# Kernel tuning notes

Hardware: AMD Instinct MI355X
Metric: run time of the kernel (lower is better)

## Reference

```python
import jax, jax.numpy as jnp
import numpy as np

DIM = 3072
NUM_HEADS = 24
HEAD_DIM = 128
INNER = NUM_HEADS * HEAD_DIM
EPS = 1e-5


def _layernorm(x, eps=EPS):
    # affine-free LayerNorm over the last (head_dim) axis
    mu = jnp.mean(x, axis=-1, keepdims=True)
    var = jnp.mean(jnp.square(x - mu), axis=-1, keepdims=True)
    return (x - mu) * jax.lax.rsqrt(var + eps)


def _rope_interleaved(x, cos, sin):
    # x: (B, S_img, H, D); cos/sin: (S_img, D//2). Non-neox (interleaved) style.
    x1 = x[..., 0::2]
    x2 = x[..., 1::2]
    c = cos[None, :, None, :]
    s = sin[None, :, None, :]
    o1 = x1 * c - x2 * s
    o2 = x2 * c + x1 * s
    return jnp.stack([o1, o2], axis=-1).reshape(x.shape)


def setup_inputs() -> dict:
    key = jax.random.key(0)
    ks = jax.random.split(key, 8)
    B, S_txt, S_img = 1, 256, 2048
    hidden_states = jax.random.normal(ks[0], (B, S_img, DIM), dtype=jnp.float32)
    encoder_hidden_states = jax.random.normal(ks[1], (B, S_txt, DIM), dtype=jnp.float32)
    cos = jax.random.uniform(ks[2], (S_img, HEAD_DIM // 2), dtype=jnp.float32)
    sin = jax.random.uniform(ks[3], (S_img, HEAD_DIM // 2), dtype=jnp.float32)
    Wqkv = jax.random.normal(ks[4], (DIM, 3 * INNER), dtype=jnp.float32) * (DIM ** -0.5)
    bqkv = jnp.zeros((3 * INNER,), dtype=jnp.float32)
    Wout = jax.random.normal(ks[5], (INNER, DIM), dtype=jnp.float32) * (INNER ** -0.5)
    bout = jnp.zeros((DIM,), dtype=jnp.float32)
    return {
        "hidden_states": hidden_states,
        "encoder_hidden_states": encoder_hidden_states,
        "cos": cos,
        "sin": sin,
        "Wqkv": Wqkv,
        "bqkv": bqkv,
        "Wout": Wout,
        "bout": bout,
        "text_seq_length": 256,
    }


def reference(hidden_states, encoder_hidden_states, cos, sin, Wqkv, bqkv, Wout, bout, text_seq_length):
    T = text_seq_length
    x = jnp.concatenate([encoder_hidden_states, hidden_states], axis=1)  # (B, S, dim)
    B, S, _ = x.shape
    qkv = x @ Wqkv + bqkv  # (B, S, 3*inner)
    q, k, v = jnp.split(qkv, 3, axis=-1)
    q = q.reshape(B, S, NUM_HEADS, HEAD_DIM)
    k = k.reshape(B, S, NUM_HEADS, HEAD_DIM)
    v = v.reshape(B, S, NUM_HEADS, HEAD_DIM)
    q = _layernorm(q)
    k = _layernorm(k)
    # partial RoPE: only on image-token slice
    q = jnp.concatenate([q[:, :T], _rope_interleaved(q[:, T:], cos, sin)], axis=1)
    k = jnp.concatenate([k[:, :T], _rope_interleaved(k[:, T:], cos, sin)], axis=1)
    scale = 1.0 / (HEAD_DIM ** 0.5)
    scores = jnp.einsum("bqhd,bkhd->bhqk", q, k) * scale
    probs = jax.nn.softmax(scores, axis=-1)
    out = jnp.einsum("bhqk,bkhd->bqhd", probs, v)
    out = out.reshape(B, S, INNER)
    out = out @ Wout + bout
    encoder_out = out[:, :T, :]
    hidden_out = out[:, T:, :]
    return (hidden_out, encoder_out)
```

## Files before the change

### kernel.cpp

```cpp
#include <hip/hip_runtime.h>

#define DIMC 3072
#define NH 24
#define HD 128
#define QKV_N 9216
#define S_TXT 256
#define S_IMG 2048
#define S_TOT 2304

typedef _Float16 f16x8 __attribute__((ext_vector_type(8)));
typedef _Float16 f16x4 __attribute__((ext_vector_type(4)));
typedef _Float16 f16x2 __attribute__((ext_vector_type(2)));
typedef float f32x4 __attribute__((ext_vector_type(4)));

#define MFMA(A, B, C) __builtin_amdgcn_mfma_f32_16x16x32_f16(A, B, C, 0, 0, 0)

#define QSCALE (0.08838834764831845f * 1.4426950408889634f)

__device__ __forceinline__ void gl2lds16(const _Float16* g, _Float16* l) {
    __builtin_amdgcn_global_load_lds(
        (const __attribute__((address_space(1))) unsigned int*)g,
        (__attribute__((address_space(3))) unsigned int*)l,
        16, 0, 0);
}

__global__ __launch_bounds__(256) void split_x(
    const float* __restrict__ enc, const float* __restrict__ hid,
    _Float16* __restrict__ xh)
{
    const int s = blockIdx.x;
    const float* src = (s < S_TXT) ? enc + (size_t)s * DIMC
                                   : hid + (size_t)(s - S_TXT) * DIMC;
    const int t = threadIdx.x;
#pragma unroll
    for (int it = 0; it < 3; ++it) {
        const int i = (it * 256 + t) * 4;
        float4 v = *(const float4*)(src + i);
        f16x4 hv;
        hv.x = (_Float16)v.x; hv.y = (_Float16)v.y;
        hv.z = (_Float16)v.z; hv.w = (_Float16)v.w;
        *(f16x4*)(xh + (size_t)s * DIMC + i) = hv;
    }
}

__global__ __launch_bounds__(256) void transpose_w_hi(
    const float* __restrict__ W, const int ldw, _Float16* __restrict__ Th)
{
    __shared__ float T[64][68];
    const int n0 = blockIdx.x * 64, k0 = blockIdx.y * 64;
    const int t = threadIdx.x;
    {
        const int r = t >> 2, c4 = (t & 3) * 16;
#pragma unroll
        for (int j = 0; j < 4; ++j) {
            float4 v = *(const float4*)(W + (size_t)(k0 + r) * ldw + n0 + c4 + j * 4);
            *(float4*)&T[r][c4 + j * 4] = v;
        }
    }
    __syncthreads();
    const int nr = t >> 2, kp = (t & 3) * 16;
    f16x8 hv0, hv1;
#pragma unroll
    for (int j = 0; j < 8; ++j) hv0[j] = (_Float16)T[kp + j][nr];
#pragma unroll
    for (int j = 0; j < 8; ++j) hv1[j] = (_Float16)T[kp + 8 + j][nr];
    _Float16* dh = Th + (size_t)(n0 + nr) * DIMC + k0 + kp;
    *(f16x8*)(dh) = hv0; *(f16x8*)(dh + 8) = hv1;
}

template <int REMAP>
__global__ __launch_bounds__(256) void gemm_f16_lds(
    const _Float16* __restrict__ Ah, const _Float16* __restrict__ Bh,
    const float* __restrict__ bias, float* __restrict__ C,
    const int nblk_m, const int ldc)
{
    __shared__ __attribute__((aligned(16))) _Float16 Ash[128 * 32];
    __shared__ __attribute__((aligned(16))) _Float16 Bsh[128 * 32];

    const int cpx = (int)gridDim.x >> 3;
    const int wgid = (blockIdx.x & 7) * cpx + (blockIdx.x >> 3);
    const int bm = (wgid % nblk_m) * 128;
    const int bn = (wgid / nblk_m) * 128;

    const int tid = threadIdx.x;
    const int l = tid & 63, w = tid >> 6;
    const int wr = w >> 1, wc = w & 1;
    const int lr = l & 15, g = l >> 4;

    const int srow0 = w * 32 + (l >> 2);
    const int srow1 = srow0 + 16;
    const int skp0 = (((l & 3) ^ ((srow0 >> 1) & 3)) * 8);
    const int skp1 = (((l & 3) ^ ((srow1 >> 1) & 3)) * 8);
    const _Float16* gA0 = Ah + (size_t)(bm + srow0) * DIMC + skp0;
    const _Float16* gA1 = Ah + (size_t)(bm + srow1) * DIMC + skp1;
    const _Float16* gB0 = Bh + (size_t)(bn + srow0) * DIMC + skp0;
    const _Float16* gB1 = Bh + (size_t)(bn + srow1) * DIMC + skp1;
    _Float16* lA0 = &Ash[(w * 32) * 32];
    _Float16* lA1 = &Ash[(w * 32 + 16) * 32];
    _Float16* lB0 = &Bsh[(w * 32) * 32];
    _Float16* lB1 = &Bsh[(w * 32 + 16) * 32];

    int aoff[4], boff[4];
#pragma unroll
    for (int i = 0; i < 4; ++i) {
        const int ra = wr * 64 + i * 16 + lr;
        const int rb = wc * 64 + i * 16 + lr;
        aoff[i] = ra * 32 + ((g ^ ((ra >> 1) & 3)) * 8);
        boff[i] = rb * 32 + ((g ^ ((rb >> 1) & 3)) * 8);
    }

    f32x4 acc[4][4] = {};

    for (int k0 = 0; k0 < DIMC; k0 += 32) {
        gl2lds16(gA0 + k0, lA0);
        gl2lds16(gA1 + k0, lA1);
        gl2lds16(gB0 + k0, lB0);
        gl2lds16(gB1 + k0, lB1);
        __syncthreads();

        f16x8 bhf[4];
#pragma unroll
        for (int ni = 0; ni < 4; ++ni)
            bhf[ni] = *(const f16x8*)&Bsh[boff[ni]];
#pragma unroll
        for (int mi = 0; mi < 4; ++mi) {
            f16x8 ahf = *(const f16x8*)&Ash[aoff[mi]];
#pragma unroll
            for (int ni = 0; ni < 4; ++ni)
                acc[mi][ni] = MFMA(ahf, bhf[ni], acc[mi][ni]);
        }
        __syncthreads();
    }

#pragma unroll
    for (int mi = 0; mi < 4; ++mi)
#pragma unroll
        for (int ni = 0; ni < 4; ++ni) {
            const int cl = bn + wc * 64 + ni * 16 + lr;
            const float bv = bias[cl];
#pragma unroll
            for (int e = 0; e < 4; ++e) {
                const int r = bm + wr * 64 + mi * 16 + g * 4 + e;
                if (REMAP) {
                    const int gr = (r < S_TXT) ? (S_IMG + r) : (r - S_TXT);
                    C[(size_t)gr * DIMC + cl] = acc[mi][ni][e] + bv;
                } else {
                    C[(size_t)r * ldc + cl] = acc[mi][ni][e] + bv;
                }
            }
        }
}

__global__ __launch_bounds__(256) void ln_rope_split(
    const float* __restrict__ qkv,
    const float* __restrict__ cost, const float* __restrict__ sint,
    _Float16* __restrict__ Qh, _Float16* __restrict__ Kh)
{
    const int wave = threadIdx.x >> 6;
    const int lane = threadIdx.x & 63;
    const int task = blockIdx.x * 4 + wave;
    const int s = task / 48;
    const int rem = task % 48;
    const int qk = rem / 24;
    const int h = rem % 24;

    const float* p = qkv + (size_t)s * QKV_N + qk * DIMC + h * HD;
    float2 x = *(const float2*)(p + lane * 2);

    float sum = x.x + x.y;
    float sq = x.x * x.x + x.y * x.y;
#pragma unroll
    for (int off = 1; off < 64; off <<= 1) {
        sum += __shfl_xor(sum, off, 64);
        sq  += __shfl_xor(sq, off, 64);
    }
    const float mu = sum * (1.0f / 128.0f);
    const float var = sq * (1.0f / 128.0f) - mu * mu;
    const float rstd = rsqrtf(var + 1e-5f);
    float y0 = (x.x - mu) * rstd;
    float y1 = (x.y - mu) * rstd;

    if (s >= S_TXT) {
        const int ip = s - S_TXT;
        const float c = cost[ip * 64 + lane];
        const float sn = sint[ip * 64 + lane];
        const float o0 = y0 * c - y1 * sn;
        const float o1 = y1 * c + y0 * sn;
        y0 = o0; y1 = o1;
    }
    if (qk == 0) { y0 *= QSCALE; y1 *= QSCALE; }

    const size_t off = ((size_t)h * S_TOT + s) * HD + lane * 2;
    f16x2 hv; hv.x = (_Float16)y0; hv.y = (_Float16)y1;
    *(f16x2*)((qk ? Kh : Qh) + off) = hv;
}

__global__ __launch_bounds__(256) void v_split_transpose(
    const float* __restrict__ qkv, _Float16* __restrict__ Vth)
{
    __shared__ float T[64][132];
    const int h = blockIdx.y;
    const int s0 = blockIdx.x * 64;
    const int t = threadIdx.x;
    {
        const int sl = t >> 2, dp = (t & 3) * 32;
#pragma unroll
        for (int j = 0; j < 8; ++j) {
            float4 v = *(const float4*)(qkv + (size_t)(s0 + sl) * QKV_N + 2 * DIMC + h * HD + dp + j * 4);
            *(float4*)&T[sl][dp + j * 4] = v;
        }
    }
    __syncthreads();
    const int d = t >> 1, sh = (t & 1) * 32;
    f16x8 hv[4];
#pragma unroll
    for (int ss = 0; ss < 32; ++ss)
        hv[ss >> 3][ss & 7] = (_Float16)T[sh + ss][d];
    _Float16* bh = Vth + ((size_t)h * HD + d) * S_TOT + s0 + sh;
#pragma unroll
    for (int j = 0; j < 4; ++j)
        *(f16x8*)(bh + j * 8) = hv[j];
}

__global__ __launch_bounds__(256) void attn_mfma(
    const _Float16* __restrict__ Qg, const _Float16* __restrict__ Kg,
    const _Float16* __restrict__ Vg, _Float16* __restrict__ aoh)
{
    __shared__ __attribute__((aligned(16))) _Float16 Ksh[4 * 64 * 32];
    __shared__ __attribute__((aligned(16))) _Float16 Vsh[128 * 64];
    __shared__ __attribute__((aligned(16))) _Float16 Pah[4 * 16 * 64];

    const int wgid = ((int)blockIdx.x & 7) * 108 + ((int)blockIdx.x >> 3);
    const int h = wgid / 36;
    const int q0 = (wgid % 36) * 64;
    const int tid = threadIdx.x;
    const int w = tid >> 6, l = tid & 63;
    const int lr = l & 15, g = l >> 4;

    const int qrow = q0 + w * 16 + lr;
    const _Float16* qb = Qg + ((size_t)h * S_TOT + qrow) * HD + g * 8;
    f16x8 qh[4];
#pragma unroll
    for (int db = 0; db < 4; ++db)
        qh[db] = *(const f16x8*)(qb + db * 32);

    f32x4 o[8] = {};
    float mrow = -3.0e38f, lrow = 0.0f;

    const int kxr = (lr >> 1) & 3;
    const int px  = lr & 7;
    int ksl[4];
#pragma unroll
    for (int db = 0; db < 4; ++db) ksl[db] = (g ^ kxr ^ db) * 8;
    const int vs0 = (g ^ px) * 8;
    const int vs1 = ((4 + g) ^ px) * 8;

    const int kkv = tid >> 2, kdb = tid & 3;
    const int vd = tid >> 1;
    const int kx = (kkv >> 1) & 3;
    const int kbase = kdb * 2048 + kkv * 32;
    const int vbase = vd * 64;
    const int vx = vd & 7;
    const int vg0 = (tid & 1) * 4;
    const _Float16* gK = Kg + ((size_t)h * S_TOT + kkv) * HD + kdb * 32;
    const _Float16* gV = Vg + ((size_t)h * HD + vd) * S_TOT + (tid & 1) * 32;

    uint4 rK0, rK1, rK2, rK3, rV0, rV1, rV2, rV3;
#define LOADKV(kv0) { \
    rK0 = *(const uint4*)(gK + (size_t)(kv0) * HD);      rK1 = *(const uint4*)(gK + (size_t)(kv0) * HD + 8); \
    rK2 = *(const uint4*)(gK + (size_t)(kv0) * HD + 16); rK3 = *(const uint4*)(gK + (size_t)(kv0) * HD + 24); \
    rV0 = *(const uint4*)(gV + (kv0));      rV1 = *(const uint4*)(gV + (kv0) + 8); \
    rV2 = *(const uint4*)(gV + (kv0) + 16); rV3 = *(const uint4*)(gV + (kv0) + 24); }

    LOADKV(0);

    for (int kb = 0; kb < S_TOT / 64; ++kb) {
        __syncthreads();
        *(uint4*)&Ksh[kbase + ((0 ^ kx ^ kdb) * 8)] = rK0;
        *(uint4*)&Ksh[kbase + ((1 ^ kx ^ kdb) * 8)] = rK1;
        *(uint4*)&Ksh[kbase + ((2 ^ kx ^ kdb) * 8)] = rK2;
        *(uint4*)&Ksh[kbase + ((3 ^ kx ^ kdb) * 8)] = rK3;
        *(uint4*)&Vsh[vbase + (((vg0 + 0) ^ vx) * 8)] = rV0;
        *(uint4*)&Vsh[vbase + (((vg0 + 1) ^ vx) * 8)] = rV1;
        *(uint4*)&Vsh[vbase + (((vg0 + 2) ^ vx) * 8)] = rV2;
        *(uint4*)&Vsh[vbase + (((vg0 + 3) ^ vx) * 8)] = rV3;
        __syncthreads();
        if (kb + 1 < S_TOT / 64) LOADKV((kb + 1) * 64);

        f32x4 sT[4] = {};
        __builtin_amdgcn_s_setprio(1);
#pragma unroll
        for (int db = 0; db < 4; ++db)
#pragma unroll
            for (int mf = 0; mf < 4; ++mf) {
                f16x8 kf = *(const f16x8*)&Ksh[db * 2048 + (mf * 16 + lr) * 32 + ksl[db]];
                sT[mf] = MFMA(kf, qh[db], sT[mf]);
            }
        __builtin_amdgcn_s_setprio(0);

        float pm = -3.0e38f;
#pragma unroll
        for (int mf = 0; mf < 4; ++mf)
#pragma unroll
            for (int e = 0; e < 4; ++e)
                pm = fmaxf(pm, sT[mf][e]);
        pm = fmaxf(pm, __shfl_xor(pm, 16, 64));
        pm = fmaxf(pm, __shfl_xor(pm, 32, 64));

        if (__any(pm > mrow + 11.0f)) {
            const float mnew = fmaxf(mrow, pm);
            const float alpha = exp2f(mrow - mnew);
            lrow *= alpha;
            mrow = mnew;
            const float a0 = __shfl(alpha, g * 4 + 0, 64);
            const float a1 = __shfl(alpha, g * 4 + 1, 64);
            const float a2 = __shfl(alpha, g * 4 + 2, 64);
            const float a3 = __shfl(alpha, g * 4 + 3, 64);
#pragma unroll
            for (int df = 0; df < 8; ++df) {
                o[df][0] *= a0; o[df][1] *= a1; o[df][2] *= a2; o[df][3] *= a3;
            }
        }

        float rs = 0.0f;
        float ex_[4][4];
#pragma unroll
        for (int mf = 0; mf < 4; ++mf)
#pragma unroll
            for (int e = 0; e < 4; ++e) {
                const float pv = exp2f(sT[mf][e] - mrow);
                ex_[mf][e] = pv;
                rs += pv;
            }
        rs += __shfl_xor(rs, 16, 64);
        rs += __shfl_xor(rs, 32, 64);
        lrow += rs;

        {
            const int pbase = w * 1024 + lr * 64;
#pragma unroll
            for (int mf = 0; mf < 4; ++mf) {
                const int slot = ((mf * 2 + (g >> 1)) ^ px) * 8 + (g & 1) * 4;
                f16x2 t0; t0.x = (_Float16)ex_[mf][0]; t0.y = (_Float16)ex_[mf][1];
                f16x2 t1; t1.x = (_Float16)ex_[mf][2]; t1.y = (_Float16)ex_[mf][3];
                *(f16x2*)&Pah[pbase + slot]     = t0;
                *(f16x2*)&Pah[pbase + slot + 2] = t1;
            }
        }

        f16x8 pa0 = *(const f16x8*)&Pah[w * 1024 + lr * 64 + vs0];
        f16x8 pa1 = *(const f16x8*)&Pah[w * 1024 + lr * 64 + vs1];
        __builtin_amdgcn_s_setprio(1);
#pragma unroll
        for (int df = 0; df < 8; ++df) {
            f16x8 vf0 = *(const f16x8*)&Vsh[(df * 16 + lr) * 64 + vs0];
            f16x8 vf1 = *(const f16x8*)&Vsh[(df * 16 + lr) * 64 + vs1];
            o[df] = MFMA(pa0, vf0, o[df]);
            o[df] = MFMA(pa1, vf1, o[df]);
        }
        __builtin_amdgcn_s_setprio(0);
    }
#undef LOADKV

    const float inv = 1.0f / lrow;
    const float b0 = __shfl(inv, g * 4 + 0, 64);
    const float b1 = __shfl(inv, g * 4 + 1, 64);
    const float b2 = __shfl(inv, g * 4 + 2, 64);
    const float b3 = __shfl(inv, g * 4 + 3, 64);
    const float bb[4] = {b0, b1, b2, b3};
#pragma unroll
    for (int df = 0; df < 8; ++df)
#pragma unroll
        for (int e = 0; e < 4; ++e) {
            const int r = q0 + w * 16 + g * 4 + e;
            aoh[(size_t)r * DIMC + h * HD + df * 16 + lr] = (_Float16)(o[df][e] * bb[e]);
        }
}

extern "C" void kernel_launch(void* const* d_in, const int* in_sizes, int n_in,
                              void* d_out, int out_size, void* d_ws, size_t ws_size,
                              hipStream_t stream)
{
    const float* hid  = (const float*)d_in[0];
    const float* enc  = (const float*)d_in[1];
    const float* cost = (const float*)d_in[2];
    const float* sint = (const float*)d_in[3];
    const float* Wqkv = (const float*)d_in[4];
    const float* bqkv = (const float*)d_in[5];
    const float* Wout = (const float*)d_in[6];
    const float* bout = (const float*)d_in[7];
    float* out = (float*)d_out;

    char* ws = (char*)d_ws;
    float*    qkv  = (float*)(ws + 0);
    _Float16* aoh  = (_Float16*)(ws + 0);
    _Float16* xh   = (_Float16*)(ws + 84934656);
    _Float16* Qh   = (_Float16*)(ws + 84934656);
    _Float16* Kh   = (_Float16*)(ws + 99090432);
    _Float16* Wth  = (_Float16*)(ws + 113246208);
    _Float16* Vth  = (_Float16*)(ws + 113246208);
    _Float16* W2h  = (_Float16*)(ws + 132120576);

    split_x<<<S_TOT, 256, 0, stream>>>(enc, hid, xh);
    transpose_w_hi<<<dim3(144, 48), 256, 0, stream>>>(Wqkv, QKV_N, Wth);
    gemm_f16_lds<0><<<18 * 72, 256, 0, stream>>>(xh, Wth, bqkv, qkv, 18, QKV_N);
    transpose_w_hi<<<dim3(48, 48), 256, 0, stream>>>(Wout, DIMC, W2h);
    ln_rope_split<<<(S_TOT * 48) / 4, 256, 0, stream>>>(qkv, cost, sint, Qh, Kh);
    v_split_transpose<<<dim3(36, 24), 256, 0, stream>>>(qkv, Vth);
    attn_mfma<<<864, 256, 0, stream>>>(Qh, Kh, Vth, aoh);
    gemm_f16_lds<1><<<18 * 24, 256, 0, stream>>>(aoh, W2h, bout, out, 18, DIMC);
}
```

Baseline: 464.1 us.

## Replace QKV GEMM with 256x256-tile double-buffered 8-wave MFMA kernel

Measured after the change: 471.7 us. About the same (+1.6%).

```diff
diff --git a/kernel.cpp b/kernel.cpp
--- a/kernel.cpp
+++ b/kernel.cpp
@@ -66,6 +66,109 @@
     for (int j = 0; j < 8; ++j) hv1[j] = (_Float16)T[kp + 8 + j][nr];
     _Float16* dh = Th + (size_t)(n0 + nr) * DIMC + k0 + kp;
     *(f16x8*)(dh) = hv0; *(f16x8*)(dh + 8) = hv1;
+}
+
+__global__ __launch_bounds__(512, 2) void gemm_f16_8ph(
+    const _Float16* __restrict__ Ah, const _Float16* __restrict__ Bh,
+    const float* __restrict__ bias, float* __restrict__ C)
+{
+    __shared__ __attribute__((aligned(16))) _Float16 lds[65536];
+
+    const int orig = blockIdx.x;
+    const int xcd = orig & 7, bidx = orig >> 3;
+    const int wgid = (xcd < 4 ? xcd * 41 : 164 + (xcd - 4) * 40) + bidx;
+    const int bm = (wgid % 9) * 256;
+    const int bn = (wgid / 9) * 256;
+
+    const int tid = threadIdx.x;
+    const int l = tid & 63, wid = tid >> 6;
+    const int wm = wid >> 2, wn = wid & 3;
+    const int lr = l & 15, g = l >> 4;
+    const int lx = lr & 7;
+
+    const int srow = tid >> 3;
+    const int sslot = tid & 7;
+    const int ldsl = (tid & 448) * 8;
+
+    const _Float16* gA[2] = { Ah + (size_t)(bm + srow) * DIMC,
+                              Ah + (size_t)(bm + 128 + srow) * DIMC };
+    const _Float16* gB[2] = { Bh + (size_t)(bn + srow) * DIMC,
+                              Bh + (size_t)(bn + 128 + srow) * DIMC };
+    const int swz0 = ((sslot ^ (srow & 7)) * 8);
+    const int swz1 = ((sslot ^ ((srow + 64) & 7)) * 8);
+
+#define STAGE_TILE(dst, k0) do { \
+    _Float16* base = &lds[(dst) * 2 * 8192]; \
+    gl2lds16(gA[0] + (k0) + swz0, base + ldsl); \
+    gl2lds16(gA[0] + (size_t)64 * DIMC + (k0) + swz1, base + 4096 + ldsl); \
+    gl2lds16(gA[1] + (k0) + swz0, base + 8192 + ldsl); \
+    gl2lds16(gA[1] + (size_t)64 * DIMC + (k0) + swz1, base + 12288 + ldsl); \
+    gl2lds16(gB[0] + (k0) + swz0, base + 32768 + ldsl); \
+    gl2lds16(gB[0] + (size_t)64 * DIMC + (k0) + swz1, base + 36864 + ldsl); \
+    gl2lds16(gB[1] + (k0) + swz0, base + 40960 + ldsl); \
+    gl2lds16(gB[1] + (size_t)64 * DIMC + (k0) + swz1, base + 45056 + ldsl); \
+} while (0)
+
+    f32x4 acc[8][4] = {};
+
+#define PHASE(d, qd) do { \
+    const int ab = ((d) * 2 + wm) * 8192; \
+    const int bb = 32768 + ((d) * 2 + (wn >> 1)) * 8192; \
+    f16x8 bf0[4], bf1[4]; \
+    _Pragma("unroll") \
+    for (int ni = 0; ni < 4; ++ni) { \
+        const int colp = (wn & 1) * 64 + ni * 16 + lr; \
+        bf0[ni] = *(const f16x8*)&lds[bb + colp * 64 + ((g ^ lx) * 8)]; \
+        bf1[ni] = *(const f16x8*)&lds[bb + colp * 64 + (((4 + g) ^ lx) * 8)]; \
+    } \
+    const int rp0 = ((qd) * 2 + 0) * 16 + lr; \
+    const int rp1 = ((qd) * 2 + 1) * 16 + lr; \
+    f16x8 a00 = *(const f16x8*)&lds[ab + rp0 * 64 + ((g ^ lx) * 8)]; \
+    f16x8 a01 = *(const f16x8*)&lds[ab + rp0 * 64 + (((4 + g) ^ lx) * 8)]; \
+    f16x8 a10 = *(const f16x8*)&lds[ab + rp1 * 64 + ((g ^ lx) * 8)]; \
+    f16x8 a11 = *(const f16x8*)&lds[ab + rp1 * 64 + (((4 + g) ^ lx) * 8)]; \
+    __builtin_amdgcn_s_setprio(1); \
+    _Pragma("unroll") \
+    for (int ni = 0; ni < 4; ++ni) { \
+        acc[(qd) * 2 + 0][ni] = MFMA(a00, bf0[ni], acc[(qd) * 2 + 0][ni]); \
+        acc[(qd) * 2 + 0][ni] = MFMA(a01, bf1[ni], acc[(qd) * 2 + 0][ni]); \
+        acc[(qd) * 2 + 1][ni] = MFMA(a10, bf0[ni], acc[(qd) * 2 + 1][ni]); \
+        acc[(qd) * 2 + 1][ni] = MFMA(a11, bf1[ni], acc[(qd) * 2 + 1][ni]); \
+    } \
+    __builtin_amdgcn_s_setprio(0); \
+} while (0)
+
+    STAGE_TILE(0, 0);
+    __syncthreads();
+
+    for (int T = 0; T < DIMC / 64; ++T) {
+        const int d = T & 1;
+        if (T + 1 < DIMC / 64) STAGE_TILE(d ^ 1, (T + 1) * 64);
+        PHASE(d, 0);
+        __builtin_amdgcn_s_barrier();
+        PHASE(d, 1);
+        __builtin_amdgcn_s_barrier();
+        PHASE(d, 2);
+        __builtin_amdgcn_s_barrier();
+        PHASE(d, 3);
+        asm volatile("s_waitcnt vmcnt(0)" ::: "memory");
+        __syncthreads();
+    }
+#undef PHASE
+#undef STAGE_TILE
+
+#pragma unroll
+    for (int mi = 0; mi < 8; ++mi)
+#pragma unroll
+        for (int ni = 0; ni < 4; ++ni) {
+            const int cl = bn + wn * 64 + ni * 16 + lr;
+            const float bv = bias[cl];
+#pragma unroll
+            for (int e = 0; e < 4; ++e) {
+                const int r = bm + wm * 128 + mi * 16 + g * 4 + e;
+                C[(size_t)r * QKV_N + cl] = acc[mi][ni][e] + bv;
+            }
+        }
 }
 
 template <int REMAP>
@@ -403,7 +506,7 @@
 
     split_x<<<S_TOT, 256, 0, stream>>>(enc, hid, xh);
     transpose_w_hi<<<dim3(144, 48), 256, 0, stream>>>(Wqkv, QKV_N, Wth);
-    gemm_f16_lds<0><<<18 * 72, 256, 0, stream>>>(xh, Wth, bqkv, qkv, 18, QKV_N);
+    gemm_f16_8ph<<<324, 512, 0, stream>>>(xh, Wth, bqkv, qkv);
     transpose_w_hi<<<dim3(48, 48), 256, 0, stream>>>(Wout, DIMC, W2h);
     ln_rope_split<<<(S_TOT * 48) / 4, 256, 0, stream>>>(qkv, cost, sint, Qh, Kh);
     v_split_transpose<<<dim3(36, 24), 256, 0, stream>>>(qkv, Vth);
```
